# Kernel optimization log

Measured on AMD Instinct MI355X. Metric: run time of the kernel, lower is better.

Reference implementation:

```python
import jax, jax.numpy as jnp
import numpy as np

D, NH, NL, NP, DFF = 256, 8, 4, 4, 1024
HD = D // NH
SHAPES = np.array([[100, 152], [50, 76], [25, 38], [13, 19]], dtype=np.int64)
LV = int((SHAPES[:, 0] * SHAPES[:, 1]).sum())  # 20197


def setup_inputs() -> dict:
    key = jax.random.key(0)
    ks = iter(jax.random.split(key, 48))
    bs, Lq = 8, 300

    def w(shape, s=0.02):
        return jax.random.normal(next(ks), shape, jnp.float32) * s

    lsi = np.concatenate([[0], np.cumsum(SHAPES[:, 0] * SHAPES[:, 1])[:-1]]).astype(np.int64)
    return dict(
        tgt=w((bs, Lq, D), 1.0),
        query_pos=w((bs, Lq, D), 1.0),
        reference_points=jax.random.uniform(next(ks), (bs, Lq, NL, 2), jnp.float32),
        src=w((bs, LV, D), 1.0),
        in_proj_w=w((3 * D, D)), in_proj_b=jnp.zeros((3 * D,), jnp.float32),
        out_proj_w=w((D, D)), out_proj_b=jnp.zeros((D,), jnp.float32),
        samp_off_w=w((NH * NL * NP * 2, D)), samp_off_b=w((NH * NL * NP * 2,), 0.5),
        attn_w_w=w((NH * NL * NP, D)), attn_w_b=jnp.zeros((NH * NL * NP,), jnp.float32),
        value_proj_w=w((D, D)), value_proj_b=jnp.zeros((D,), jnp.float32),
        output_proj_w=w((D, D)), output_proj_b=jnp.zeros((D,), jnp.float32),
        lin1_w=w((DFF, D)), lin1_b=jnp.zeros((DFF,), jnp.float32),
        lin2_w=w((D, DFF)), lin2_b=jnp.zeros((D,), jnp.float32),
        norm1_w=jnp.ones((D,), jnp.float32), norm1_b=jnp.zeros((D,), jnp.float32),
        norm2_w=jnp.ones((D,), jnp.float32), norm2_b=jnp.zeros((D,), jnp.float32),
        norm3_w=jnp.ones((D,), jnp.float32), norm3_b=jnp.zeros((D,), jnp.float32),
        spatial_shapes=SHAPES,            # static numpy (shapes must be static)
        level_start_index=lsi,            # static numpy
        padding_mask=jnp.zeros((bs, LV), bool),
    )


def _ln(x, w, b):
    m = x.mean(-1, keepdims=True)
    v = ((x - m) ** 2).mean(-1, keepdims=True)
    return (x - m) * jax.lax.rsqrt(v + 1e-5) * w + b


def _bilinear(vflat, H_, W_, loc):
    # vflat: (b,h,H*W,d); loc: (b,h,q,p,2) normalized to [0,1]
    # matches F.grid_sample(align_corners=False, padding_mode='zeros')
    x = loc[..., 0] * W_ - 0.5
    y = loc[..., 1] * H_ - 0.5
    x0f, y0f = jnp.floor(x), jnp.floor(y)
    lx, ly = x - x0f, y - y0f
    x0, y0 = x0f.astype(jnp.int32), y0f.astype(jnp.int32)
    b, h, q, p = x0.shape

    def gather(ix, iy, wgt):
        valid = (ix >= 0) & (ix < W_) & (iy >= 0) & (iy < H_)
        idx = (jnp.clip(iy, 0, H_ - 1) * W_ + jnp.clip(ix, 0, W_ - 1)).reshape(b, h, q * p)
        g = jnp.take_along_axis(vflat, idx[..., None], axis=2)  # (b,h,q*p,d)
        return g * (wgt * valid).reshape(b, h, q * p, 1)

    out = (gather(x0, y0, (1 - lx) * (1 - ly)) + gather(x0 + 1, y0, lx * (1 - ly))
           + gather(x0, y0 + 1, (1 - lx) * ly) + gather(x0 + 1, y0 + 1, lx * ly))
    return out.reshape(b, h, q, p, -1)


def reference(tgt, query_pos, reference_points, src, in_proj_w, in_proj_b,
              out_proj_w, out_proj_b, samp_off_w, samp_off_b, attn_w_w, attn_w_b,
              value_proj_w, value_proj_b, output_proj_w, output_proj_b,
              lin1_w, lin1_b, lin2_w, lin2_b, norm1_w, norm1_b, norm2_w, norm2_b,
              norm3_w, norm3_b, spatial_shapes, level_start_index, padding_mask):
    bs, Lq, _ = tgt.shape
    ss = np.asarray(spatial_shapes)
    lsi = np.asarray(level_start_index)

    # ---- self attention (eval mode, dropout off) ----
    qk = tgt + query_pos
    qh = (qk @ in_proj_w[:D].T + in_proj_b[:D]).reshape(bs, Lq, NH, HD)
    kh = (qk @ in_proj_w[D:2 * D].T + in_proj_b[D:2 * D]).reshape(bs, Lq, NH, HD)
    vh = (tgt @ in_proj_w[2 * D:].T + in_proj_b[2 * D:]).reshape(bs, Lq, NH, HD)
    scores = jnp.einsum('bqhd,bkhd->bhqk', qh, kh) / jnp.sqrt(jnp.float32(HD))
    attn = jax.nn.softmax(scores, axis=-1)
    sa = jnp.einsum('bhqk,bkhd->bqhd', attn, vh).reshape(bs, Lq, D)
    sa = sa @ out_proj_w.T + out_proj_b
    x = _ln(tgt + sa, norm2_w, norm2_b)

    # ---- MSDeformAttn cross attention ----
    query = x + query_pos
    value = src @ value_proj_w.T + value_proj_b
    value = jnp.where(padding_mask[..., None], 0.0, value)
    value_t = value.reshape(bs, -1, NH, HD).transpose(0, 2, 1, 3)  # (b,h,Lv,d)

    offsets = (query @ samp_off_w.T + samp_off_b).reshape(bs, Lq, NH, NL, NP, 2)
    aw = jax.nn.softmax((query @ attn_w_w.T + attn_w_b).reshape(bs, Lq, NH, NL * NP), -1)
    aw = aw.reshape(bs, Lq, NH, NL, NP)
    norma = jnp.asarray(np.stack([ss[:, 1], ss[:, 0]], -1), jnp.float32)  # (NL,2)=[W,H]
    loc = reference_points[:, :, None, :, None, :] + offsets / norma[None, None, None, :, None, :]

    out = jnp.zeros((bs, Lq, NH, HD), value.dtype)
    for l in range(NL):
        H_, W_ = int(ss[l, 0]), int(ss[l, 1])
        s0 = int(lsi[l])
        vl = value_t[:, :, s0:s0 + H_ * W_]                    # (b,h,HW,d)
        ll = loc[:, :, :, l].transpose(0, 2, 1, 3, 4)          # (b,h,q,p,2)
        samp = _bilinear(vl, H_, W_, ll)                       # (b,h,q,p,d)
        out = out + jnp.einsum('bhqpd,bqhp->bqhd', samp, aw[:, :, :, l])
    ca = out.reshape(bs, Lq, D) @ output_proj_w.T + output_proj_b
    x = _ln(x + ca, norm1_w, norm1_b)

    # ---- FFN ----
    ffn = jax.nn.relu(x @ lin1_w.T + lin1_b) @ lin2_w.T + lin2_b
    x = _ln(x + ffn, norm3_w, norm3_b)
    return (x, loc, aw)
```

## Files before the change

kernel.cpp:

```cpp
#include <hip/hip_runtime.h>
#include <hip/hip_bf16.h>

#define D_ 256
#define NH_ 8
#define HD_ 32
#define NL_ 4
#define NP_ 4
#define DFF_ 1024
#define BS_ 8
#define LQ_ 300
#define LV_ 20197
#define NQ_ (BS_*LQ_)
#define NSRC_ (BS_*LV_*D_)

__device__ __forceinline__ float u2f(unsigned int u) {
    union { unsigned int i; float f; } v; v.i = u << 16; return v.f;
}
__device__ __forceinline__ float lo2f(unsigned int u) {
    union { unsigned int i; float f; } v; v.i = u << 16; return v.f;
}
__device__ __forceinline__ float hi2f(unsigned int u) {
    union { unsigned int i; float f; } v; v.i = u & 0xffff0000u; return v.f;
}
__device__ __forceinline__ unsigned short f2bf_bits(float f) {
    __hip_bfloat16 b = __float2bfloat16(f);
    union { __hip_bfloat16 b; unsigned short u; } v; v.b = b; return v.u;
}

#define DOT4(accum, wv, ap) do { \
    float4 _a = *(const float4*)(ap); \
    accum += wv.x*_a.x + wv.y*_a.y + wv.z*_a.z + wv.w*_a.w; } while(0)

__global__ __launch_bounds__(256) void cvt_bf16_kernel(
    const float* __restrict__ src, const float* __restrict__ wv,
    unsigned short* __restrict__ vbf, unsigned short* __restrict__ wbf)
{
    const int nsrc4 = NSRC_/4;
    const int total4 = nsrc4 + (D_*D_)/4;
    for (int i = blockIdx.x*256 + threadIdx.x; i < total4; i += gridDim.x*256) {
        float4 v;
        if (i < nsrc4) v = ((const float4*)src)[i];
        else           v = ((const float4*)wv)[i - nsrc4];
        ushort4 o;
        o.x = f2bf_bits(v.x); o.y = f2bf_bits(v.y);
        o.z = f2bf_bits(v.z); o.w = f2bf_bits(v.w);
        if (i < nsrc4) ((ushort4*)vbf)[i] = o;
        else           ((ushort4*)wbf)[i - nsrc4] = o;
    }
}

__global__ __launch_bounds__(256) void qkv_kernel(
    const float* __restrict__ tgt, const float* __restrict__ qp,
    const float* __restrict__ w, const float* __restrict__ bias,
    float* __restrict__ qh, float* __restrict__ kh, float* __restrict__ vh)
{
    __shared__ float arow[8][D_];
    const int t = threadIdx.x, m0 = blockIdx.x * 8, pass = blockIdx.y;
    for (int r = 0; r < 8; ++r) {
        float tv = tgt[(m0+r)*D_ + t];
        arow[r][t] = (pass == 2) ? tv : tv + qp[(m0+r)*D_ + t];
    }
    __syncthreads();
    const float4* w4 = (const float4*)(w + (pass*256 + t)*D_);
    float acc[8] = {0,0,0,0,0,0,0,0};
    for (int c = 0; c < 64; ++c) {
        float4 wv = w4[c];
#pragma unroll
        for (int r = 0; r < 8; ++r) DOT4(acc[r], wv, &arow[r][c*4]);
    }
    float bb = bias[pass*256 + t];
    float* dst = (pass == 0) ? qh : (pass == 1) ? kh : vh;
    for (int r = 0; r < 8; ++r) dst[(m0+r)*D_ + t] = acc[r] + bb;
}

__global__ __launch_bounds__(256) void attn_kernel(
    const float* __restrict__ qh, const float* __restrict__ kh,
    const float* __restrict__ vh, float* __restrict__ sa)
{
    __shared__ unsigned short khl[LQ_][HD_+2];
    __shared__ unsigned short vhl[LQ_][HD_+2];
    __shared__ float sc[4][LQ_];
    __shared__ float qbuf[4][HD_];
    const int b = blockIdx.x >> 3, h = blockIdx.x & 7, chunk = blockIdx.y;
    const int t = threadIdx.x, w = t >> 6, lane = t & 63;
    for (int i = t; i < LQ_*HD_; i += 256) {
        int kq = i >> 5, d = i & 31;
        khl[kq][d] = f2bf_bits(kh[(b*LQ_ + kq)*D_ + h*HD_ + d]);
        vhl[kq][d] = f2bf_bits(vh[(b*LQ_ + kq)*D_ + h*HD_ + d]);
    }
    __syncthreads();
    const float scale = 0.17677669529663687f;
    for (int qi = 0; qi < 15; ++qi) {
        const int q = chunk*60 + w*15 + qi;
        if (lane < HD_) qbuf[w][lane] = qh[(b*LQ_ + q)*D_ + h*HD_ + lane];
        float qv[HD_];
#pragma unroll
        for (int d2 = 0; d2 < HD_; ++d2) qv[d2] = qbuf[w][d2];
        float mx = -1e30f;
        for (int k = lane; k < LQ_; k += 64) {
            float s = 0.f;
#pragma unroll
            for (int d2 = 0; d2 < HD_; ++d2) s += qv[d2]*u2f(khl[k][d2]);
            s *= scale;
            sc[w][k] = s;
            mx = fmaxf(mx, s);
        }
#pragma unroll
        for (int off = 32; off; off >>= 1) mx = fmaxf(mx, __shfl_xor(mx, off));
        float lsum = 0.f;
        for (int k = lane; k < LQ_; k += 64) {
            float e = __expf(sc[w][k] - mx);
            sc[w][k] = e; lsum += e;
        }
#pragma unroll
        for (int off = 32; off; off >>= 1) lsum += __shfl_xor(lsum, off);
        const int d = lane & 31, half = lane >> 5;
        float acc = 0.f;
        for (int k = half*150; k < half*150 + 150; ++k) acc += sc[w][k]*u2f(vhl[k][d]);
        acc += __shfl_down(acc, 32);
        if (lane < 32) sa[(b*LQ_ + q)*D_ + h*HD_ + d] = acc / lsum;
    }
}

__global__ __launch_bounds__(256) void proj_res_ln_kernel(
    const float* __restrict__ A, const float* __restrict__ W,
    const float* __restrict__ bias, const float* __restrict__ res,
    const float* __restrict__ gw, const float* __restrict__ gb,
    float* __restrict__ out)
{
    __shared__ float arow[8][D_];
    __shared__ float2 part[4][8];
    const int t = threadIdx.x, m0 = blockIdx.x * 8;
    const int w = t >> 6, lane = t & 63;
    for (int r = 0; r < 8; ++r) arow[r][t] = A[(m0+r)*D_ + t];
    __syncthreads();
    float acc[8] = {0,0,0,0,0,0,0,0};
    const float4* w4 = (const float4*)(W + t*D_);
    for (int c = 0; c < 64; ++c) {
        float4 wv = w4[c];
#pragma unroll
        for (int r = 0; r < 8; ++r) DOT4(acc[r], wv, &arow[r][c*4]);
    }
    const float bb = bias[t], gwv = gw[t], gbv = gb[t];
    float v[8];
#pragma unroll
    for (int r = 0; r < 8; ++r) {
        v[r] = acc[r] + bb + res[(m0+r)*D_+t];
        float s = v[r], ss = v[r]*v[r];
#pragma unroll
        for (int off = 32; off; off >>= 1) {
            s += __shfl_xor(s, off); ss += __shfl_xor(ss, off);
        }
        if (lane == 0) part[w][r] = make_float2(s, ss);
    }
    __syncthreads();
#pragma unroll
    for (int r = 0; r < 8; ++r) {
        float2 p0 = part[0][r], p1 = part[1][r], p2 = part[2][r], p3 = part[3][r];
        float mean = (p0.x+p1.x+p2.x+p3.x) * (1.0f/256.0f);
        float ex2  = (p0.y+p1.y+p2.y+p3.y) * (1.0f/256.0f);
        float var  = ex2 - mean*mean;
        out[(m0+r)*D_+t] = (v[r]-mean) * rsqrtf(var + 1e-5f) * gwv + gbv;
    }
}

__global__ __launch_bounds__(256) void samp_params_kernel(
    const float* __restrict__ x1, const float* __restrict__ qp,
    const float* __restrict__ so_w, const float* __restrict__ so_b,
    const float* __restrict__ aw_w, const float* __restrict__ aw_b,
    const float* __restrict__ refp,
    float* __restrict__ loc_out, float* __restrict__ aw_out)
{
    __shared__ float qrow[8][D_];
    __shared__ float logits[8][128];
    const int t = threadIdx.x, m0 = blockIdx.x * 8;
    for (int r = 0; r < 8; ++r)
        qrow[r][t] = x1[(m0+r)*D_ + t] + qp[(m0+r)*D_ + t];
    __syncthreads();
    {
        float acc[8] = {0,0,0,0,0,0,0,0};
        const float4* w4 = (const float4*)(so_w + t*D_);
        for (int c = 0; c < 64; ++c) {
            float4 wv = w4[c];
#pragma unroll
            for (int r = 0; r < 8; ++r) DOT4(acc[r], wv, &qrow[r][c*4]);
        }
        const float ob = so_b[t];
        const int c_ = t & 1, l_ = (t >> 3) & 3;
        float nrm;
        if (c_ == 0) nrm = (l_==0)?152.f:(l_==1)?76.f:(l_==2)?38.f:19.f;
        else         nrm = (l_==0)?100.f:(l_==1)?50.f:(l_==2)?25.f:13.f;
        for (int r = 0; r < 8; ++r) {
            int m = m0 + r;
            float off = acc[r] + ob;
            loc_out[m*256 + t] = refp[(m*NL_ + l_)*2 + c_] + off / nrm;
        }
    }
    if (t < 128) {
        float acc[8] = {0,0,0,0,0,0,0,0};
        const float4* w4 = (const float4*)(aw_w + t*D_);
        for (int c = 0; c < 64; ++c) {
            float4 wv = w4[c];
#pragma unroll
            for (int r = 0; r < 8; ++r) DOT4(acc[r], wv, &qrow[r][c*4]);
        }
        const float ab = aw_b[t];
        for (int r = 0; r < 8; ++r) logits[r][t] = acc[r] + ab;
    }
    __syncthreads();
    if (t < 128) {
        const int g0 = (t >> 4) << 4;
        for (int r = 0; r < 8; ++r) {
            float mx = -1e30f;
            for (int j = 0; j < 16; ++j) mx = fmaxf(mx, logits[r][g0+j]);
            float s = 0.f;
            for (int j = 0; j < 16; ++j) s += __expf(logits[r][g0+j] - mx);
            aw_out[(m0+r)*128 + t] = __expf(logits[r][t] - mx) / s;
        }
    }
}

__global__ __launch_bounds__(256) void samp_fuse_bf16_kernel(
    const unsigned short* __restrict__ vbf,
    const float* __restrict__ loc_f, const float* __restrict__ aw_f,
    float* __restrict__ svec_g, float* __restrict__ wsum_g)
{
    __shared__ int   cidx[128][4];
    __shared__ float cwt[128][4];
    const int m = blockIdx.x, t = threadIdx.x;
    const int b = m / LQ_;

    if (t < 128) {
        const int l = (t >> 2) & 3;
        const int HS[4] = {100,50,25,13}, WS[4] = {152,76,38,19}, S0[4] = {0,15200,19000,19950};
        const int Hh = HS[l], Ww = WS[l], s0 = S0[l];
        const float aw = aw_f[m*128 + t];
        const float x = loc_f[m*256 + 2*t]*Ww - 0.5f;
        const float y = loc_f[m*256 + 2*t + 1]*Hh - 0.5f;
        const float x0f = floorf(x), y0f = floorf(y);
        const int x0 = (int)x0f, y0 = (int)y0f;
        const float fx = x - x0f, fy = y - y0f;
        const int   cx[4] = {x0, x0+1, x0,   x0+1};
        const int   cy[4] = {y0, y0,   y0+1, y0+1};
        const float cw[4] = {(1.f-fx)*(1.f-fy), fx*(1.f-fy), (1.f-fx)*fy, fx*fy};
        float sw = 0.f;
#pragma unroll
        for (int j = 0; j < 4; ++j) {
            const bool valid = (cx[j] >= 0) & (cx[j] < Ww) & (cy[j] >= 0) & (cy[j] < Hh);
            cidx[t][j] = valid ? (s0 + cy[j]*Ww + cx[j]) : s0;
            float wv = valid ? aw*cw[j] : 0.f;
            cwt[t][j] = wv;
            sw += wv;
        }
#pragma unroll
        for (int off = 8; off; off >>= 1) sw += __shfl_xor(sw, off);
        if ((t & 15) == 0) wsum_g[m*NH_ + (t >> 4)] = sw;
    }
    __syncthreads();

    const int hh = (t >> 7) * 4;
    const int c  = t & 127;
    const unsigned int* sb = (const unsigned int*)(vbf + (size_t)b*LV_*D_) + c;
#pragma unroll
    for (int h = hh; h < hh + 4; ++h) {
        float e0=0.f, e1=0.f, e2=0.f, e3=0.f;
        float o0=0.f, o1=0.f, o2=0.f, o3=0.f;
#pragma unroll 4
        for (int s = 0; s < 16; ++s) {
            const int base = h*16 + s;
            const int   i0 = cidx[base][0], i1 = cidx[base][1],
                        i2 = cidx[base][2], i3 = cidx[base][3];
            const float w0 = cwt[base][0], w1 = cwt[base][1],
                        w2 = cwt[base][2], w3 = cwt[base][3];
            const unsigned int u0 = sb[(size_t)i0*128];
            const unsigned int u1 = sb[(size_t)i1*128];
            const unsigned int u2 = sb[(size_t)i2*128];
            const unsigned int u3 = sb[(size_t)i3*128];
            e0 += w0*lo2f(u0); o0 += w0*hi2f(u0);
            e1 += w1*lo2f(u1); o1 += w1*hi2f(u1);
            e2 += w2*lo2f(u2); o2 += w2*hi2f(u2);
            e3 += w3*lo2f(u3); o3 += w3*hi2f(u3);
        }
        *(float2*)&svec_g[(size_t)m*(NH_*D_) + h*D_ + 2*c] =
            make_float2((e0+e1)+(e2+e3), (o0+o1)+(o2+o3));
    }
}

__global__ __launch_bounds__(256) void vproj_kernel(
    const float* __restrict__ svec_g, const float* __restrict__ wsum_g,
    const unsigned short* __restrict__ wbf, const float* __restrict__ vpb,
    float* __restrict__ vo)
{
    __shared__ float sv[4][NH_*D_];
    const int t = threadIdx.x, m0 = blockIdx.x * 4;
    for (int i = t; i < 4*NH_*D_; i += 256)
        sv[i >> 11][i & 2047] = svec_g[(size_t)m0*(NH_*D_) + i];
    __syncthreads();
    const int h = t >> 5;
    const ushort4* w4 = (const ushort4*)(wbf + t*D_);
    float a0 = 0.f, a1 = 0.f, a2 = 0.f, a3 = 0.f;
    for (int c = 0; c < 64; ++c) {
        const ushort4 wq = w4[c];
        const float wx = u2f(wq.x), wy = u2f(wq.y), wz = u2f(wq.z), ww = u2f(wq.w);
        const float4 s0 = *(const float4*)&sv[0][h*D_ + c*4];
        const float4 s1 = *(const float4*)&sv[1][h*D_ + c*4];
        const float4 s2 = *(const float4*)&sv[2][h*D_ + c*4];
        const float4 s3 = *(const float4*)&sv[3][h*D_ + c*4];
        a0 += wx*s0.x + wy*s0.y + wz*s0.z + ww*s0.w;
        a1 += wx*s1.x + wy*s1.y + wz*s1.z + ww*s1.w;
        a2 += wx*s2.x + wy*s2.y + wz*s2.z + ww*s2.w;
        a3 += wx*s3.x + wy*s3.y + wz*s3.z + ww*s3.w;
    }
    const float bb = vpb[t];
    vo[(size_t)(m0+0)*D_ + t] = a0 + bb*wsum_g[(m0+0)*NH_ + h];
    vo[(size_t)(m0+1)*D_ + t] = a1 + bb*wsum_g[(m0+1)*NH_ + h];
    vo[(size_t)(m0+2)*D_ + t] = a2 + bb*wsum_g[(m0+2)*NH_ + h];
    vo[(size_t)(m0+3)*D_ + t] = a3 + bb*wsum_g[(m0+3)*NH_ + h];
}

__global__ __launch_bounds__(256) void samp_fuse_f32_kernel(
    const float* __restrict__ src, const float* __restrict__ Wv,
    const float* __restrict__ vpb,
    const float* __restrict__ loc_f, const float* __restrict__ aw_f,
    float* __restrict__ vo)
{
    __shared__ float svec[NH_][D_];
    __shared__ int   cidx[128][4];
    __shared__ float cwt[128][4];
    __shared__ float wsum[NH_];
    const int m = blockIdx.x, t = threadIdx.x;
    const int b = m / LQ_;

    if (t < 128) {
        const int l = (t >> 2) & 3;
        const int HS[4] = {100,50,25,13}, WS[4] = {152,76,38,19}, S0[4] = {0,15200,19000,19950};
        const int Hh = HS[l], Ww = WS[l], s0 = S0[l];
        const float aw = aw_f[m*128 + t];
        const float x = loc_f[m*256 + 2*t]*Ww - 0.5f;
        const float y = loc_f[m*256 + 2*t + 1]*Hh - 0.5f;
        const float x0f = floorf(x), y0f = floorf(y);
        const int x0 = (int)x0f, y0 = (int)y0f;
        const float fx = x - x0f, fy = y - y0f;
        const int   cx[4] = {x0, x0+1, x0,   x0+1};
        const int   cy[4] = {y0, y0,   y0+1, y0+1};
        const float cw[4] = {(1.f-fx)*(1.f-fy), fx*(1.f-fy), (1.f-fx)*fy, fx*fy};
        float sw = 0.f;
#pragma unroll
        for (int jj = 0; jj < 4; ++jj) {
            const bool valid = (cx[jj] >= 0) & (cx[jj] < Ww) & (cy[jj] >= 0) & (cy[jj] < Hh);
            cidx[t][jj] = valid ? (s0 + cy[jj]*Ww + cx[jj]) : s0;
            float wv = valid ? aw*cw[jj] : 0.f;
            cwt[t][jj] = wv;
            sw += wv;
        }
#pragma unroll
        for (int off = 8; off; off >>= 1) sw += __shfl_xor(sw, off);
        if ((t & 15) == 0) wsum[t >> 4] = sw;
    }
    __syncthreads();

    const float* sb = src + (size_t)b*LV_*D_ + t;
#pragma unroll
    for (int h = 0; h < NH_; ++h) {
        float a0 = 0.f, a1 = 0.f, a2 = 0.f, a3 = 0.f;
#pragma unroll 4
        for (int s = 0; s < 16; ++s) {
            const int base = h*16 + s;
            const int   i0 = cidx[base][0], i1 = cidx[base][1],
                        i2 = cidx[base][2], i3 = cidx[base][3];
            const float w0 = cwt[base][0], w1 = cwt[base][1],
                        w2 = cwt[base][2], w3 = cwt[base][3];
            a0 += w0 * sb[(size_t)i0*D_];
            a1 += w1 * sb[(size_t)i1*D_];
            a2 += w2 * sb[(size_t)i2*D_];
            a3 += w3 * sb[(size_t)i3*D_];
        }
        svec[h][t] = (a0 + a1) + (a2 + a3);
    }
    __syncthreads();

    const int h = t >> 5;
    const float4* w4 = (const float4*)(Wv + t*D_);
    float a = 0.f;
    for (int c = 0; c < 64; ++c) {
        float4 wv = w4[c];
        DOT4(a, wv, &svec[h][c*4]);
    }
    vo[m*D_ + t] = a + vpb[t]*wsum[h];
}

__global__ __launch_bounds__(256) void ffn1_kernel(
    const float* __restrict__ x2, const float* __restrict__ W1,
    const float* __restrict__ b1, float* __restrict__ hid)
{
    __shared__ float arow[8][D_];
    const int t = threadIdx.x, m0 = blockIdx.x * 8, cc = blockIdx.y;
    for (int r = 0; r < 8; ++r) arow[r][t] = x2[(m0+r)*D_ + t];
    __syncthreads();
    const int j = cc*256 + t;
    float acc[8] = {0,0,0,0,0,0,0,0};
    const float4* w4 = (const float4*)(W1 + j*D_);
    for (int c = 0; c < 64; ++c) {
        float4 wv = w4[c];
#pragma unroll
        for (int r = 0; r < 8; ++r) DOT4(acc[r], wv, &arow[r][c*4]);
    }
    const float bb = b1[j];
    for (int r = 0; r < 8; ++r) {
        float v = acc[r] + bb;
        hid[(m0+r)*DFF_ + j] = v > 0.f ? v : 0.f;
    }
}

__global__ __launch_bounds__(256) void ffn2_ln_kernel(
    const float* __restrict__ hid, const float* __restrict__ W2,
    const float* __restrict__ b2, const float* __restrict__ res,
    const float* __restrict__ gw, const float* __restrict__ gb,
    float* __restrict__ out)
{
    __shared__ float hrow[8][DFF_];
    __shared__ float2 part[4][8];
    const int t = threadIdx.x, m0 = blockIdx.x * 8;
    const int w = t >> 6, lane = t & 63;
    for (int i = t; i < 8*DFF_; i += 256)
        hrow[i >> 10][i & 1023] = hid[(m0 + (i >> 10))*DFF_ + (i & 1023)];
    __syncthreads();
    float acc[8] = {0,0,0,0,0,0,0,0};
    const float4* w4 = (const float4*)(W2 + t*DFF_);
    for (int c = 0; c < 256; ++c) {
        float4 wv = w4[c];
#pragma unroll
        for (int r = 0; r < 8; ++r) DOT4(acc[r], wv, &hrow[r][c*4]);
    }
    const float bb = b2[t], gwv = gw[t], gbv = gb[t];
    float v[8];
#pragma unroll
    for (int r = 0; r < 8; ++r) {
        v[r] = acc[r] + bb + res[(m0+r)*D_+t];
        float s = v[r], ss = v[r]*v[r];
#pragma unroll
        for (int off = 32; off; off >>= 1) {
            s += __shfl_xor(s, off); ss += __shfl_xor(ss, off);
        }
        if (lane == 0) part[w][r] = make_float2(s, ss);
    }
    __syncthreads();
#pragma unroll
    for (int r = 0; r < 8; ++r) {
        float2 p0 = part[0][r], p1 = part[1][r], p2 = part[2][r], p3 = part[3][r];
        float mean = (p0.x+p1.x+p2.x+p3.x) * (1.0f/256.0f);
        float ex2  = (p0.y+p1.y+p2.y+p3.y) * (1.0f/256.0f);
        float var  = ex2 - mean*mean;
        out[(m0+r)*D_+t] = (v[r]-mean) * rsqrtf(var + 1e-5f) * gwv + gbv;
    }
}

extern "C" void kernel_launch(void* const* d_in, const int* in_sizes, int n_in,
                              void* d_out, int out_size, void* d_ws, size_t ws_size,
                              hipStream_t stream) {
    (void)in_sizes; (void)n_in; (void)out_size;
    const float* tgt  = (const float*)d_in[0];
    const float* qpos = (const float*)d_in[1];
    const float* refp = (const float*)d_in[2];
    const float* srcp = (const float*)d_in[3];
    const float* ipw  = (const float*)d_in[4];
    const float* ipb  = (const float*)d_in[5];
    const float* opw  = (const float*)d_in[6];
    const float* opb  = (const float*)d_in[7];
    const float* sow  = (const float*)d_in[8];
    const float* sob  = (const float*)d_in[9];
    const float* aww  = (const float*)d_in[10];
    const float* awb  = (const float*)d_in[11];
    const float* vpw  = (const float*)d_in[12];
    const float* vpb  = (const float*)d_in[13];
    const float* outw = (const float*)d_in[14];
    const float* outb = (const float*)d_in[15];
    const float* l1w  = (const float*)d_in[16];
    const float* l1b  = (const float*)d_in[17];
    const float* l2w  = (const float*)d_in[18];
    const float* l2b  = (const float*)d_in[19];
    const float* n1w  = (const float*)d_in[20];
    const float* n1b  = (const float*)d_in[21];
    const float* n2w  = (const float*)d_in[22];
    const float* n2b  = (const float*)d_in[23];
    const float* n3w  = (const float*)d_in[24];
    const float* n3b  = (const float*)d_in[25];

    float* wsf = (float*)d_ws;
    float* qh   = wsf;
    float* kh   = wsf + 614400;
    float* vh   = wsf + 1228800;
    float* sa   = wsf + 1843200;
    float* x1   = wsf + 2457600;
    float* vo   = wsf + 3072000;
    float* x2   = wsf + 3686400;
    float* hid  = wsf + 4300800;
    unsigned short* vbf = (unsigned short*)(wsf + 6758400);
    unsigned short* wbf = (unsigned short*)(wsf + 6758400 + 20681728);
    float* svec_g = wsf + 6758400 + 20681728 + 32768;
    float* wsum_g = svec_g + 4915200;
    const size_t need_bytes = (size_t)(6758400 + 20681728 + 32768 + 4915200 + 19200) * 4;
    const bool use_bf16 = ws_size >= need_bytes;

    float* xout   = (float*)d_out;
    float* locout = xout + 614400;
    float* awout  = xout + 1228800;

    if (use_bf16)
        cvt_bf16_kernel<<<2048, 256, 0, stream>>>(srcp, vpw, vbf, wbf);
    qkv_kernel<<<dim3(NQ_/8, 3), 256, 0, stream>>>(tgt, qpos, ipw, ipb, qh, kh, vh);
    attn_kernel<<<dim3(BS_*NH_, 5), 256, 0, stream>>>(qh, kh, vh, sa);
    proj_res_ln_kernel<<<NQ_/8, 256, 0, stream>>>(sa, opw, opb, tgt, n2w, n2b, x1);
    samp_params_kernel<<<NQ_/8, 256, 0, stream>>>(x1, qpos, sow, sob, aww, awb, refp,
                                                  locout, awout);
    if (use_bf16) {
        samp_fuse_bf16_kernel<<<NQ_, 256, 0, stream>>>(vbf, locout, awout, svec_g, wsum_g);
        vproj_kernel<<<NQ_/4, 256, 0, stream>>>(svec_g, wsum_g, wbf, vpb, vo);
    } else {
        samp_fuse_f32_kernel<<<NQ_, 256, 0, stream>>>(srcp, vpw, vpb, locout, awout, vo);
    }
    proj_res_ln_kernel<<<NQ_/8, 256, 0, stream>>>(vo, outw, outb, x1, n1w, n1b, x2);
    ffn1_kernel<<<dim3(NQ_/8, 4), 256, 0, stream>>>(x2, l1w, l1b, hid);
    ffn2_ln_kernel<<<NQ_/8, 256, 0, stream>>>(hid, l2w, l2b, x2, n3w, n3b, xout);
}
```

Baseline: 654.7 us.

## Transpose all weight matrices into float4-interleaved layout for coalesced GEMV loads

Adds a kernel that transposes every linear weight matrix into a layout where consecutive threads read consecutive float4s for the same input chunk, and switches all projection kernels to strided-by-output indexing. Previously each thread read its own contiguous row, so a wavefront's loads spanned many cache lines per instruction. The value-projection weight is now kept in fp32 instead of bf16. This adds a transpose pass over all weights on every call plus extra workspace.

```diff
diff --git a/kernel.cpp b/kernel.cpp
--- a/kernel.cpp
+++ b/kernel.cpp
@@ -32,26 +32,55 @@
     accum += wv.x*_a.x + wv.y*_a.y + wv.z*_a.z + wv.w*_a.w; } while(0)
 
 __global__ __launch_bounds__(256) void cvt_bf16_kernel(
-    const float* __restrict__ src, const float* __restrict__ wv,
-    unsigned short* __restrict__ vbf, unsigned short* __restrict__ wbf)
+    const float* __restrict__ src, unsigned short* __restrict__ vbf)
 {
     const int nsrc4 = NSRC_/4;
-    const int total4 = nsrc4 + (D_*D_)/4;
-    for (int i = blockIdx.x*256 + threadIdx.x; i < total4; i += gridDim.x*256) {
-        float4 v;
-        if (i < nsrc4) v = ((const float4*)src)[i];
-        else           v = ((const float4*)wv)[i - nsrc4];
+    for (int i = blockIdx.x*256 + threadIdx.x; i < nsrc4; i += gridDim.x*256) {
+        float4 v = ((const float4*)src)[i];
         ushort4 o;
         o.x = f2bf_bits(v.x); o.y = f2bf_bits(v.y);
         o.z = f2bf_bits(v.z); o.w = f2bf_bits(v.w);
-        if (i < nsrc4) ((ushort4*)vbf)[i] = o;
-        else           ((ushort4*)wbf)[i - nsrc4] = o;
-    }
+        ((ushort4*)vbf)[i] = o;
+    }
+}
+
+__global__ __launch_bounds__(256) void pack_weights_kernel(
+    const float4* __restrict__ ipw,  const float4* __restrict__ opw,
+    const float4* __restrict__ sow,  const float4* __restrict__ aww,
+    const float4* __restrict__ outw, const float4* __restrict__ l1w,
+    const float4* __restrict__ l2w,  const float4* __restrict__ vpw,
+    float4* __restrict__ ipwP,  float4* __restrict__ opwP,
+    float4* __restrict__ sowP,  float4* __restrict__ awwP,
+    float4* __restrict__ outwP, float4* __restrict__ l1wP,
+    float4* __restrict__ l2wP,  float4* __restrict__ vpwP)
+{
+    __shared__ float4 tile[32][33];
+    const int RS[8]  = {768,256,256,128,256,1024,256,256};
+    const int C4S[8] = {64, 64, 64, 64, 64, 64, 256, 64};
+    const int TCUM[9] = {0,48,64,80,88,104,168,232,248};
+    int tb = blockIdx.x, mi = 0;
+    while (tb >= TCUM[mi+1]) ++mi;
+    const int lt = tb - TCUM[mi];
+    const float4* in  = (mi==0)?ipw :(mi==1)?opw :(mi==2)?sow :(mi==3)?aww
+                       :(mi==4)?outw:(mi==5)?l1w :(mi==6)?l2w :vpw;
+    float4* out       = (mi==0)?ipwP:(mi==1)?opwP:(mi==2)?sowP:(mi==3)?awwP
+                       :(mi==4)?outwP:(mi==5)?l1wP:(mi==6)?l2wP:vpwP;
+    const int R = RS[mi], C4 = C4S[mi];
+    const int tpr = C4 >> 5;
+    const int by = lt / tpr, bx = lt % tpr;
+    const int tx = threadIdx.x & 31, ty = threadIdx.x >> 5;
+#pragma unroll
+    for (int i = 0; i < 32; i += 8)
+        tile[ty+i][tx] = in[(size_t)(by*32+ty+i)*C4 + bx*32+tx];
+    __syncthreads();
+#pragma unroll
+    for (int i = 0; i < 32; i += 8)
+        out[(size_t)(bx*32+ty+i)*R + by*32+tx] = tile[tx][ty+i];
 }
 
 __global__ __launch_bounds__(256) void qkv_kernel(
     const float* __restrict__ tgt, const float* __restrict__ qp,
-    const float* __restrict__ w, const float* __restrict__ bias,
+    const float4* __restrict__ ipwP, const float* __restrict__ bias,
     float* __restrict__ qh, float* __restrict__ kh, float* __restrict__ vh)
 {
     __shared__ float arow[8][D_];
@@ -61,10 +90,10 @@
         arow[r][t] = (pass == 2) ? tv : tv + qp[(m0+r)*D_ + t];
     }
     __syncthreads();
-    const float4* w4 = (const float4*)(w + (pass*256 + t)*D_);
+    const float4* w4 = ipwP + pass*256 + t;
     float acc[8] = {0,0,0,0,0,0,0,0};
     for (int c = 0; c < 64; ++c) {
-        float4 wv = w4[c];
+        float4 wv = w4[c*768];
 #pragma unroll
         for (int r = 0; r < 8; ++r) DOT4(acc[r], wv, &arow[r][c*4]);
     }
@@ -123,7 +152,7 @@
 }
 
 __global__ __launch_bounds__(256) void proj_res_ln_kernel(
-    const float* __restrict__ A, const float* __restrict__ W,
+    const float* __restrict__ A, const float4* __restrict__ WP,
     const float* __restrict__ bias, const float* __restrict__ res,
     const float* __restrict__ gw, const float* __restrict__ gb,
     float* __restrict__ out)
@@ -135,9 +164,9 @@
     for (int r = 0; r < 8; ++r) arow[r][t] = A[(m0+r)*D_ + t];
     __syncthreads();
     float acc[8] = {0,0,0,0,0,0,0,0};
-    const float4* w4 = (const float4*)(W + t*D_);
+    const float4* w4 = WP + t;
     for (int c = 0; c < 64; ++c) {
-        float4 wv = w4[c];
+        float4 wv = w4[c*256];
 #pragma unroll
         for (int r = 0; r < 8; ++r) DOT4(acc[r], wv, &arow[r][c*4]);
     }
@@ -166,8 +195,8 @@
 
 __global__ __launch_bounds__(256) void samp_params_kernel(
     const float* __restrict__ x1, const float* __restrict__ qp,
-    const float* __restrict__ so_w, const float* __restrict__ so_b,
-    const float* __restrict__ aw_w, const float* __restrict__ aw_b,
+    const float4* __restrict__ sowP, const float* __restrict__ so_b,
+    const float4* __restrict__ awwP, const float* __restrict__ aw_b,
     const float* __restrict__ refp,
     float* __restrict__ loc_out, float* __restrict__ aw_out)
 {
@@ -179,9 +208,9 @@
     __syncthreads();
     {
         float acc[8] = {0,0,0,0,0,0,0,0};
-        const float4* w4 = (const float4*)(so_w + t*D_);
+        const float4* w4 = sowP + t;
         for (int c = 0; c < 64; ++c) {
-            float4 wv = w4[c];
+            float4 wv = w4[c*256];
 #pragma unroll
             for (int r = 0; r < 8; ++r) DOT4(acc[r], wv, &qrow[r][c*4]);
         }
@@ -198,9 +227,9 @@
     }
     if (t < 128) {
         float acc[8] = {0,0,0,0,0,0,0,0};
-        const float4* w4 = (const float4*)(aw_w + t*D_);
+        const float4* w4 = awwP + t;
         for (int c = 0; c < 64; ++c) {
-            float4 wv = w4[c];
+            float4 wv = w4[c*128];
 #pragma unroll
             for (int r = 0; r < 8; ++r) DOT4(acc[r], wv, &qrow[r][c*4]);
         }
@@ -288,7 +317,7 @@
 
 __global__ __launch_bounds__(256) void vproj_kernel(
     const float* __restrict__ svec_g, const float* __restrict__ wsum_g,
-    const unsigned short* __restrict__ wbf, const float* __restrict__ vpb,
+    const float4* __restrict__ vpwP, const float* __restrict__ vpb,
     float* __restrict__ vo)
 {
     __shared__ float sv[4][NH_*D_];
@@ -297,19 +326,18 @@
         sv[i >> 11][i & 2047] = svec_g[(size_t)m0*(NH_*D_) + i];
     __syncthreads();
     const int h = t >> 5;
-    const ushort4* w4 = (const ushort4*)(wbf + t*D_);
+    const float4* w4 = vpwP + t;
     float a0 = 0.f, a1 = 0.f, a2 = 0.f, a3 = 0.f;
     for (int c = 0; c < 64; ++c) {
-        const ushort4 wq = w4[c];
-        const float wx = u2f(wq.x), wy = u2f(wq.y), wz = u2f(wq.z), ww = u2f(wq.w);
+        const float4 wq = w4[c*256];
         const float4 s0 = *(const float4*)&sv[0][h*D_ + c*4];
         const float4 s1 = *(const float4*)&sv[1][h*D_ + c*4];
         const float4 s2 = *(const float4*)&sv[2][h*D_ + c*4];
         const float4 s3 = *(const float4*)&sv[3][h*D_ + c*4];
-        a0 += wx*s0.x + wy*s0.y + wz*s0.z + ww*s0.w;
-        a1 += wx*s1.x + wy*s1.y + wz*s1.z + ww*s1.w;
-        a2 += wx*s2.x + wy*s2.y + wz*s2.z + ww*s2.w;
-        a3 += wx*s3.x + wy*s3.y + wz*s3.z + ww*s3.w;
+        a0 += wq.x*s0.x + wq.y*s0.y + wq.z*s0.z + wq.w*s0.w;
+        a1 += wq.x*s1.x + wq.y*s1.y + wq.z*s1.z + wq.w*s1.w;
+        a2 += wq.x*s2.x + wq.y*s2.y + wq.z*s2.z + wq.w*s2.w;
+        a3 += wq.x*s3.x + wq.y*s3.y + wq.z*s3.z + wq.w*s3.w;
     }
     const float bb = vpb[t];
     vo[(size_t)(m0+0)*D_ + t] = a0 + bb*wsum_g[(m0+0)*NH_ + h];
@@ -390,7 +418,7 @@
 }
 
 __global__ __launch_bounds__(256) void ffn1_kernel(
-    const float* __restrict__ x2, const float* __restrict__ W1,
+    const float* __restrict__ x2, const float4* __restrict__ l1wP,
     const float* __restrict__ b1, float* __restrict__ hid)
 {
     __shared__ float arow[8][D_];
@@ -399,9 +427,9 @@
     __syncthreads();
     const int j = cc*256 + t;
     float acc[8] = {0,0,0,0,0,0,0,0};
-    const float4* w4 = (const float4*)(W1 + j*D_);
+    const float4* w4 = l1wP + j;
     for (int c = 0; c < 64; ++c) {
-        float4 wv = w4[c];
+        float4 wv = w4[c*1024];
 #pragma unroll
         for (int r = 0; r < 8; ++r) DOT4(acc[r], wv, &arow[r][c*4]);
     }
@@ -413,7 +441,7 @@
 }
 
 __global__ __launch_bounds__(256) void ffn2_ln_kernel(
-    const float* __restrict__ hid, const float* __restrict__ W2,
+    const float* __restrict__ hid, const float4* __restrict__ l2wP,
     const float* __restrict__ b2, const float* __restrict__ res,
     const float* __restrict__ gw, const float* __restrict__ gb,
     float* __restrict__ out)
@@ -426,9 +454,9 @@
         hrow[i >> 10][i & 1023] = hid[(m0 + (i >> 10))*DFF_ + (i & 1023)];
     __syncthreads();
     float acc[8] = {0,0,0,0,0,0,0,0};
-    const float4* w4 = (const float4*)(W2 + t*DFF_);
+    const float4* w4 = l2wP + t;
     for (int c = 0; c < 256; ++c) {
-        float4 wv = w4[c];
+        float4 wv = w4[c*256];
 #pragma unroll
         for (int r = 0; r < 8; ++r) DOT4(acc[r], wv, &hrow[r][c*4]);
     }
@@ -495,31 +523,44 @@
     float* vo   = wsf + 3072000;
     float* x2   = wsf + 3686400;
     float* hid  = wsf + 4300800;
-    unsigned short* vbf = (unsigned short*)(wsf + 6758400);
-    unsigned short* wbf = (unsigned short*)(wsf + 6758400 + 20681728);
-    float* svec_g = wsf + 6758400 + 20681728 + 32768;
+    float* P0    = wsf + 6758400;
+    float4* ipwP  = (float4*)(P0);
+    float4* opwP  = (float4*)(P0 + 196608);
+    float4* sowP  = (float4*)(P0 + 262144);
+    float4* awwP  = (float4*)(P0 + 327680);
+    float4* outwP = (float4*)(P0 + 360448);
+    float4* l1wP  = (float4*)(P0 + 425984);
+    float4* l2wP  = (float4*)(P0 + 688128);
+    float4* vpwP  = (float4*)(P0 + 950272);
+    unsigned short* vbf = (unsigned short*)(wsf + 7774208);
+    float* svec_g = wsf + 7774208 + 20681728;
     float* wsum_g = svec_g + 4915200;
-    const size_t need_bytes = (size_t)(6758400 + 20681728 + 32768 + 4915200 + 19200) * 4;
+    const size_t need_bytes = (size_t)(7774208 + 20681728 + 4915200 + 19200) * 4;
     const bool use_bf16 = ws_size >= need_bytes;
 
     float* xout   = (float*)d_out;
     float* locout = xout + 614400;
     float* awout  = xout + 1228800;
 
+    pack_weights_kernel<<<248, 256, 0, stream>>>(
+        (const float4*)ipw, (const float4*)opw, (const float4*)sow,
+        (const float4*)aww, (const float4*)outw, (const float4*)l1w,
+        (const float4*)l2w, (const float4*)vpw,
+        ipwP, opwP, sowP, awwP, outwP, l1wP, l2wP, vpwP);
     if (use_bf16)
-        cvt_bf16_kernel<<<2048, 256, 0, stream>>>(srcp, vpw, vbf, wbf);
-    qkv_kernel<<<dim3(NQ_/8, 3), 256, 0, stream>>>(tgt, qpos, ipw, ipb, qh, kh, vh);
+        cvt_bf16_kernel<<<2048, 256, 0, stream>>>(srcp, vbf);
+    qkv_kernel<<<dim3(NQ_/8, 3), 256, 0, stream>>>(tgt, qpos, ipwP, ipb, qh, kh, vh);
     attn_kernel<<<dim3(BS_*NH_, 5), 256, 0, stream>>>(qh, kh, vh, sa);
-    proj_res_ln_kernel<<<NQ_/8, 256, 0, stream>>>(sa, opw, opb, tgt, n2w, n2b, x1);
-    samp_params_kernel<<<NQ_/8, 256, 0, stream>>>(x1, qpos, sow, sob, aww, awb, refp,
+    proj_res_ln_kernel<<<NQ_/8, 256, 0, stream>>>(sa, opwP, opb, tgt, n2w, n2b, x1);
+    samp_params_kernel<<<NQ_/8, 256, 0, stream>>>(x1, qpos, sowP, sob, awwP, awb, refp,
                                                   locout, awout);
     if (use_bf16) {
         samp_fuse_bf16_kernel<<<NQ_, 256, 0, stream>>>(vbf, locout, awout, svec_g, wsum_g);
-        vproj_kernel<<<NQ_/4, 256, 0, stream>>>(svec_g, wsum_g, wbf, vpb, vo);
+        vproj_kernel<<<NQ_/4, 256, 0, stream>>>(svec_g, wsum_g, vpwP, vpb, vo);
     } else {
         samp_fuse_f32_kernel<<<NQ_, 256, 0, stream>>>(srcp, vpw, vpb, locout, awout, vo);
     }
-    proj_res_ln_kernel<<<NQ_/8, 256, 0, stream>>>(vo, outw, outb, x1, n1w, n1b, x2);
-    ffn1_kernel<<<dim3(NQ_/8, 4), 256, 0, stream>>>(x2, l1w, l1b, hid);
-    ffn2_ln_kernel<<<NQ_/8, 256, 0, stream>>>(hid, l2w, l2b, x2, n3w, n3b, xout);
-}
+    proj_res_ln_kernel<<<NQ_/8, 256, 0, stream>>>(vo, outwP, outb, x1, n1w, n1b, x2);
+    ffn1_kernel<<<dim3(NQ_/8, 4), 256, 0, stream>>>(x2, l1wP, l1b, hid);
+    ffn2_ln_kernel<<<NQ_/8, 256, 0, stream>>>(hid, l2wP, l2b, x2, n3w, n3b, xout);
+}
```

Measured after the change: 673.7 us. 1.03x slower.
